# Kernel optimization log

Measured on AMD Instinct MI355X. Metric: run time of the kernel, lower is better.

## Reference

```python
import jax, jax.numpy as jnp
import numpy as np

D = 128
NHEAD = 4
HD = D // NHEAD
DFF = 2 * D
K = 3
NL = 2


def _ln(x, g, b, eps=1e-5):
    m = jnp.mean(x, axis=-1, keepdims=True)
    v = jnp.var(x, axis=-1, keepdims=True)
    return (x - m) / jnp.sqrt(v + eps) * g + b


def setup_inputs() -> dict:
    key = jax.random.key(0)
    ks = jax.random.split(key, 20)
    B, C, H, W = 2, 16, 128, 128
    inp = {
        "x": jax.random.normal(ks[0], (B, C, H, W), jnp.float32),
        "emb_w": jax.random.normal(ks[1], (D, C), jnp.float32) * (1.0 / np.sqrt(C)),
        "emb_b": jnp.zeros((D,), jnp.float32),
        "pos": jax.random.normal(ks[2], (1, K * K, D), jnp.float32) * 0.02,
        "wqkv": jax.random.normal(ks[3], (NL, 3 * D, D), jnp.float32) * (1.0 / np.sqrt(D)),
        "bqkv": jnp.zeros((NL, 3 * D), jnp.float32),
        "wo": jax.random.normal(ks[4], (NL, D, D), jnp.float32) * (1.0 / np.sqrt(D)),
        "bo": jnp.zeros((NL, D), jnp.float32),
        "ln1_g": jnp.ones((NL, D), jnp.float32),
        "ln1_b": jnp.zeros((NL, D), jnp.float32),
        "ln2_g": jnp.ones((NL, D), jnp.float32),
        "ln2_b": jnp.zeros((NL, D), jnp.float32),
        "w1": jax.random.normal(ks[5], (NL, DFF, D), jnp.float32) * (1.0 / np.sqrt(D)),
        "b1": jnp.zeros((NL, DFF), jnp.float32),
        "w2": jax.random.normal(ks[6], (NL, D, DFF), jnp.float32) * (1.0 / np.sqrt(DFF)),
        "b2": jnp.zeros((NL, D), jnp.float32),
        "lnf_g": jnp.ones((D,), jnp.float32),
        "lnf_b": jnp.zeros((D,), jnp.float32),
        "head_w": jax.random.normal(ks[7], (1, D), jnp.float32) * (1.0 / np.sqrt(D)),
        "head_b": jnp.zeros((1,), jnp.float32),
    }
    return inp


def reference(x, emb_w, emb_b, pos, wqkv, bqkv, wo, bo, ln1_g, ln1_b,
              ln2_g, ln2_b, w1, b1, w2, b2, lnf_g, lnf_b, head_w, head_b):
    B, C, H, W = x.shape
    # 1x1 conv embedding -> (B,H,W,D)
    e = jnp.einsum('bchw,dc->bhwd', x, emb_w) + emb_b
    # unfold: 3x3 windows with padding 1, kernel positions in row-major order
    ep = jnp.pad(e, ((0, 0), (1, 1), (1, 1), (0, 0)))
    wins = jnp.stack([ep[:, i:i + H, j:j + W, :]
                      for i in range(K) for j in range(K)], axis=3)  # (B,H,W,9,D)
    t = wins.reshape(B * H * W, K * K, D) + pos[0]  # (N,9,D)
    scale = 1.0 / np.sqrt(HD)

    def split_heads(a):
        return a.reshape(-1, K * K, NHEAD, HD).transpose(0, 2, 1, 3)

    for l in range(NL):
        # pre-LN self-attention
        h = _ln(t, ln1_g[l], ln1_b[l])
        qkv = h @ wqkv[l].T + bqkv[l]            # (N,9,3D)
        q, k, v = jnp.split(qkv, 3, axis=-1)
        q, k, v = split_heads(q), split_heads(k), split_heads(v)
        att = jax.nn.softmax(jnp.einsum('nhqd,nhkd->nhqk', q, k) * scale, axis=-1)
        o = jnp.einsum('nhqk,nhkd->nhqd', att, v)
        o = o.transpose(0, 2, 1, 3).reshape(-1, K * K, D)
        t = t + o @ wo[l].T + bo[l]
        # pre-LN FFN with exact GELU
        h2 = _ln(t, ln2_g[l], ln2_b[l])
        t = t + jax.nn.gelu(h2 @ w1[l].T + b1[l], approximate=False) @ w2[l].T + b2[l]

    center = t[:, (K * K) // 2, :]               # (N,D)
    center = _ln(center, lnf_g, lnf_b)
    logits = center @ head_w.T + head_b          # (N,1)
    return logits.reshape(B, H, W, 1).transpose(0, 3, 1, 2)
```

## Files before the change

kernel.cpp:

```cpp
#include <hip/hip_runtime.h>
#include <hip/hip_bf16.h>

typedef unsigned short u16;
typedef unsigned int   u32;
typedef __attribute__((ext_vector_type(8))) short bf16x8;
typedef __attribute__((ext_vector_type(4))) float f32x4;
typedef __attribute__((ext_vector_type(2))) unsigned int u32x2;

#define NTOK 32768
#define TPB  4
#define MR   36
#define MPAD 48
#define NBLK (NTOK/TPB)

#define QK_OFF 0
#define VT_OFF 24576
#define HB_OFF 40960
#define SM_ATTN 53248

__device__ __forceinline__ u16 f2bf(float f) {
    u32 u; __builtin_memcpy(&u, &f, 4);
    u32 r = (u + 0x7fffu + ((u >> 16) & 1u)) >> 16;
    return (u16)r;
}
__device__ __forceinline__ u32 packbf2(float a, float b) {
    __hip_bfloat162 h = __float22bfloat162_rn(make_float2(a, b));
    u32 r; __builtin_memcpy(&r, &h, 4); return r;
}
__device__ __forceinline__ float wredsum(float v) {
#pragma unroll
    for (int m = 32; m >= 1; m >>= 1) v += __shfl_xor(v, m, 64);
    return v;
}
__device__ __forceinline__ float gelu_f(float x) {
    float ax = fabsf(x) * 0.70710678118654752f;
    float tt = __builtin_amdgcn_rcpf(1.0f + 0.3275911f * ax);
    float poly = tt * (0.254829592f + tt * (-0.284496736f + tt * (1.421413741f +
                 tt * (-1.453152027f + tt * 1.061405429f))));
    float er = 1.0f - poly * __expf(-ax * ax);
    er = copysignf(er, x);
    return 0.5f * x * (1.0f + er);
}

__global__ __launch_bounds__(256) void k_wconv(const float* __restrict__ wqkv, const float* __restrict__ wo,
                                               const float* __restrict__ w1, const float* __restrict__ w2,
                                               u16* __restrict__ wbf) {
    int i = blockIdx.x * 256 + threadIdx.x;
    float v;
    if (i < 98304)       v = wqkv[i];
    else if (i < 131072) v = wo[i - 98304];
    else if (i < 196608) v = w1[i - 131072];
    else                 v = w2[i - 196608];
    wbf[i] = f2bf(v);
}

__global__ __launch_bounds__(256) void k_embed(const float* __restrict__ x, const float* __restrict__ ew,
                                               const float* __restrict__ eb, float* __restrict__ e) {
    int idx = blockIdx.x * 256 + threadIdx.x;
    int d = idx & 127, pix = idx >> 7;
    int b = pix >> 14, hw = pix & 16383;
    const float* xp = x + b * 262144 + hw;
    const float* wr = ew + d * 16;
    float acc = eb[d];
#pragma unroll
    for (int c = 0; c < 16; ++c) acc += xp[c * 16384] * wr[c];
    e[idx] = acc;
}

__global__ __launch_bounds__(256) void k_build(const float* __restrict__ e, const float* __restrict__ pos,
                                               float* __restrict__ t) {
    int id = blockIdx.x * 256 + threadIdx.x;
    int c4 = (id & 31) << 2;
    int np = id >> 5;
    int p = np % 9;
    int n = np / 9;
    int b = n >> 14, h = (n >> 7) & 127, w = n & 127;
    int sh = h + p / 3 - 1, sw = w + p % 3 - 1;
    float4 v = {0.f, 0.f, 0.f, 0.f};
    if (sh >= 0 && sh < 128 && sw >= 0 && sw < 128)
        v = *(const float4*)(e + (size_t)((b << 14) + (sh << 7) + sw) * 128 + c4);
    float4 pv = *(const float4*)(pos + p * 128 + c4);
    v.x += pv.x; v.y += pv.y; v.z += pv.z; v.w += pv.w;
    *(float4*)(t + (size_t)np * 128 + c4) = v;
}

__global__ __launch_bounds__(512, 6) void k_attn(
    float* __restrict__ t,
    const u16* __restrict__ wq, const float* __restrict__ bq,
    const u16* __restrict__ wov, const float* __restrict__ bov,
    const float* __restrict__ lg, const float* __restrict__ lb) {
    __shared__ char smem[SM_ATTN];
    char* qk = smem + QK_OFF;
    char* vt = smem + VT_OFF;
    char* hb = smem + HB_OFF;
    const int tid = threadIdx.x, lane = tid & 63, wid = tid >> 6;
    const int blk = blockIdx.x;
    const int col = lane & 15, grp = lane >> 4;
    const f32x4 zero4 = {0.f, 0.f, 0.f, 0.f};

    *(f32x4*)(vt + tid * 32) = zero4;
    *(f32x4*)(vt + tid * 32 + 16) = zero4;
    if (tid < 192) {
        int pr = MR + (tid >> 4), pc = (tid & 15) * 16;
        *(f32x4*)(hb + pr * 256 + (pc ^ ((pr & 7) << 4))) = zero4;
    }
    {
        float2 gv = ((const float2*)lg)[lane];
        float2 bv = ((const float2*)lb)[lane];
        for (int r = wid; r < MR; r += 8) {
            const float2* tr = (const float2*)(t + ((size_t)blk * MR + r) * 128);
            float2 xv = tr[lane];
            float mean = wredsum(xv.x + xv.y) * (1.f / 128.f);
            float var  = wredsum(xv.x * xv.x + xv.y * xv.y) * (1.f / 128.f) - mean * mean;
            float rstd = rsqrtf(var + 1e-5f);
            float h0 = (xv.x - mean) * rstd * gv.x + bv.x;
            float h1 = (xv.y - mean) * rstd * gv.y + bv.y;
            *(u32*)(hb + r * 256 + ((lane * 4) ^ ((r & 7) << 4))) = packbf2(h0, h1);
        }
    }
    __syncthreads();
    for (int nt = 0; nt < 3; ++nt) {
        int n0 = (wid * 3 + nt) * 16;
        int nr = n0 + col;
        bf16x8 bfr[4];
        const u16* wr = wq + nr * 128 + grp * 8;
#pragma unroll
        for (int ks = 0; ks < 4; ++ks) bfr[ks] = *(const bf16x8*)(wr + ks * 32);
        if (n0 < 256) {
            float scl = (n0 < 128) ? 0.17677669529663687f : 1.0f;
            float4 b4 = *(const float4*)(bq + n0 + grp * 4);
            for (int mt = 0; mt < 3; ++mt) {
                f32x4 acc = zero4;
#pragma unroll
                for (int ks = 0; ks < 4; ++ks) {
                    int row = mt * 16 + col;
                    bf16x8 a = *(const bf16x8*)(hb + row * 256 + ((ks * 64 + grp * 16) ^ ((row & 7) << 4)));
                    acc = __builtin_amdgcn_mfma_f32_16x16x32_bf16(bfr[ks], a, acc, 0, 0, 0);
                }
                int R = mt * 16 + col;
                u32x2 pk;
                pk.x = packbf2((acc[0] + b4.x) * scl, (acc[1] + b4.y) * scl);
                pk.y = packbf2((acc[2] + b4.z) * scl, (acc[3] + b4.w) * scl);
                *(u32x2*)(qk + R * 512 + (((n0 + grp * 4) * 2) ^ ((R & 7) << 4))) = pk;
            }
        } else {
            float bias = bq[nr];
            for (int mt = 0; mt < 3; ++mt) {
                f32x4 acc = zero4;
#pragma unroll
                for (int ks = 0; ks < 4; ++ks) {
                    int row = mt * 16 + col;
                    bf16x8 a = *(const bf16x8*)(hb + row * 256 + ((ks * 64 + grp * 16) ^ ((row & 7) << 4)));
                    acc = __builtin_amdgcn_mfma_f32_16x16x32_bf16(a, bfr[ks], acc, 0, 0, 0);
                }
#pragma unroll
                for (int j = 0; j < 4; ++j) {
                    int R = mt * 16 + grp * 4 + j;
                    if (R < MR) {
                        int tok = R / 9, jp = R % 9;
                        int d = nr - 256;
                        *(u16*)(vt + tok * 4096 + (jp >> 3) * 2048 + d * 16 + (jp & 7) * 2) = f2bf(acc[j] + bias);
                    }
                }
            }
        }
    }
    __syncthreads();
    for (int i = 0; i < 2; ++i) {
        int pair = wid * 2 + i;
        int tok = pair >> 2, head = pair & 3;
        int rb = tok * 9;
        int rm = rb + (col < 9 ? col : 8);
        bf16x8 kf = *(const bf16x8*)(qk + rm * 512 + ((256 + head * 64 + grp * 16) ^ ((rm & 7) << 4)));
        bf16x8 qf = *(const bf16x8*)(qk + rm * 512 + ((head * 64 + grp * 16) ^ ((rm & 7) << 4)));
        f32x4 s = __builtin_amdgcn_mfma_f32_16x16x32_bf16(kf, qf, zero4, 0, 0, 0);
        int jb = grp * 4;
        float mx = -1e30f;
#pragma unroll
        for (int r = 0; r < 4; ++r) if (jb + r < 9) mx = fmaxf(mx, s[r]);
        mx = fmaxf(mx, __shfl_xor(mx, 16, 64));
        mx = fmaxf(mx, __shfl_xor(mx, 32, 64));
        float e0[4], ss = 0.f;
#pragma unroll
        for (int r = 0; r < 4; ++r) { e0[r] = (jb + r < 9) ? __expf(s[r] - mx) : 0.f; ss += e0[r]; }
        ss += __shfl_xor(ss, 16, 64);
        ss += __shfl_xor(ss, 32, 64);
        float rinv = __builtin_amdgcn_rcpf(ss);
        u32 p0 = packbf2(e0[0] * rinv, e0[1] * rinv);
        u32 p1 = packbf2(e0[2] * rinv, e0[3] * rinv);
        int idx0 = (col + 32 * grp) * 4;
        u32 w0 = (u32)__builtin_amdgcn_ds_bpermute(idx0, (int)p0);
        u32 w1 = (u32)__builtin_amdgcn_ds_bpermute(idx0, (int)p1);
        u32 w2 = (u32)__builtin_amdgcn_ds_bpermute(idx0 + 64, (int)p0);
        u32 w3 = (u32)__builtin_amdgcn_ds_bpermute(idx0 + 64, (int)p1);
        if (grp >= 2) { w0 = 0; w1 = 0; w2 = 0; w3 = 0; }
        union { u32 w[4]; bf16x8 v; } bu;
        bu.w[0] = w0; bu.w[1] = w1; bu.w[2] = w2; bu.w[3] = w3;
#pragma unroll
        for (int dh = 0; dh < 2; ++dh) {
            bf16x8 af = *(const bf16x8*)(vt + tok * 4096 + (grp & 1) * 2048 + (head * 32 + dh * 16 + col) * 16);
            f32x4 o = __builtin_amdgcn_mfma_f32_16x16x32_bf16(af, bu.v, zero4, 0, 0, 0);
            if (col < 9) {
                int row = rb + col;
                u32x2 pk; pk.x = packbf2(o[0], o[1]); pk.y = packbf2(o[2], o[3]);
                *(u32x2*)(hb + row * 256 + ((head * 64 + dh * 32 + grp * 8) ^ ((row & 7) << 4))) = pk;
            }
        }
    }
    __syncthreads();
    {
        int n0w = wid * 16;
        int nr = n0w + col;
        bf16x8 bw[4];
        const u16* wr = wov + nr * 128 + grp * 8;
#pragma unroll
        for (int ks = 0; ks < 4; ++ks) bw[ks] = *(const bf16x8*)(wr + ks * 32);
        float4 b4 = *(const float4*)(bov + n0w + grp * 4);
        for (int mt = 0; mt < 3; ++mt) {
            f32x4 acc = zero4;
#pragma unroll
            for (int ks = 0; ks < 4; ++ks) {
                int row = mt * 16 + col;
                bf16x8 a = *(const bf16x8*)(hb + row * 256 + ((ks * 64 + grp * 16) ^ ((row & 7) << 4)));
                acc = __builtin_amdgcn_mfma_f32_16x16x32_bf16(bw[ks], a, acc, 0, 0, 0);
            }
            int R = mt * 16 + col;
            if (R < MR) {
                float* p = t + ((size_t)blk * MR + R) * 128 + n0w + grp * 4;
                float4 old = *(float4*)p;
                old.x += acc[0] + b4.x; old.y += acc[1] + b4.y;
                old.z += acc[2] + b4.z; old.w += acc[3] + b4.w;
                *(float4*)p = old;
            }
        }
    }
}

__global__ __launch_bounds__(512, 6) void k_ffn(
    float* __restrict__ t,
    const u16* __restrict__ w1w, const float* __restrict__ b1v,
    const u16* __restrict__ w2w, const float* __restrict__ b2v,
    const float* __restrict__ lg, const float* __restrict__ lb) {
    __shared__ char smem[36864];
    char* hb  = smem;
    char* mid = smem + 12288;
    const int tid = threadIdx.x, lane = tid & 63, wid = tid >> 6;
    const int blk = blockIdx.x;
    const int col = lane & 15, grp = lane >> 4;
    const f32x4 zero4 = {0.f, 0.f, 0.f, 0.f};

    if (tid < 192) {
        int pr = MR + (tid >> 4), pc = (tid & 15) * 16;
        *(f32x4*)(hb + pr * 256 + (pc ^ ((pr & 7) << 4))) = zero4;
    }
    {
        float2 gv = ((const float2*)lg)[lane];
        float2 bv = ((const float2*)lb)[lane];
        for (int r = wid; r < MR; r += 8) {
            const float2* tr = (const float2*)(t + ((size_t)blk * MR + r) * 128);
            float2 xv = tr[lane];
            float mean = wredsum(xv.x + xv.y) * (1.f / 128.f);
            float var  = wredsum(xv.x * xv.x + xv.y * xv.y) * (1.f / 128.f) - mean * mean;
            float rstd = rsqrtf(var + 1e-5f);
            float h0 = (xv.x - mean) * rstd * gv.x + bv.x;
            float h1 = (xv.y - mean) * rstd * gv.y + bv.y;
            *(u32*)(hb + r * 256 + ((lane * 4) ^ ((r & 7) << 4))) = packbf2(h0, h1);
        }
    }
    __syncthreads();
    for (int nt = 0; nt < 2; ++nt) {
        int n0 = (wid * 2 + nt) * 16;
        int nr = n0 + col;
        bf16x8 bfr[4];
        const u16* wr = w1w + nr * 128 + grp * 8;
#pragma unroll
        for (int ks = 0; ks < 4; ++ks) bfr[ks] = *(const bf16x8*)(wr + ks * 32);
        float4 b4 = *(const float4*)(b1v + n0 + grp * 4);
        for (int mt = 0; mt < 3; ++mt) {
            f32x4 acc = zero4;
#pragma unroll
            for (int ks = 0; ks < 4; ++ks) {
                int row = mt * 16 + col;
                bf16x8 a = *(const bf16x8*)(hb + row * 256 + ((ks * 64 + grp * 16) ^ ((row & 7) << 4)));
                acc = __builtin_amdgcn_mfma_f32_16x16x32_bf16(bfr[ks], a, acc, 0, 0, 0);
            }
            int R = mt * 16 + col;
            float g0 = gelu_f(acc[0] + b4.x), g1 = gelu_f(acc[1] + b4.y);
            float g2 = gelu_f(acc[2] + b4.z), g3 = gelu_f(acc[3] + b4.w);
            u32x2 pk; pk.x = packbf2(g0, g1); pk.y = packbf2(g2, g3);
            *(u32x2*)(mid + R * 512 + (((n0 + grp * 4) * 2) ^ ((R & 7) << 4))) = pk;
        }
    }
    __syncthreads();
    {
        int n0w = wid * 16;
        int nr = n0w + col;
        bf16x8 bfr[8];
        const u16* wr = w2w + nr * 256 + grp * 8;
#pragma unroll
        for (int ks = 0; ks < 8; ++ks) bfr[ks] = *(const bf16x8*)(wr + ks * 32);
        float4 b4 = *(const float4*)(b2v + n0w + grp * 4);
        for (int mt = 0; mt < 3; ++mt) {
            f32x4 acc = zero4;
#pragma unroll
            for (int ks = 0; ks < 8; ++ks) {
                int row = mt * 16 + col;
                bf16x8 a = *(const bf16x8*)(mid + row * 512 + ((ks * 64 + grp * 16) ^ ((row & 7) << 4)));
                acc = __builtin_amdgcn_mfma_f32_16x16x32_bf16(bfr[ks], a, acc, 0, 0, 0);
            }
            int R = mt * 16 + col;
            if (R < MR) {
                float* p = t + ((size_t)blk * MR + R) * 128 + n0w + grp * 4;
                float4 old = *(float4*)p;
                old.x += acc[0] + b4.x; old.y += acc[1] + b4.y;
                old.z += acc[2] + b4.z; old.w += acc[3] + b4.w;
                *(float4*)p = old;
            }
        }
    }
}

__global__ __launch_bounds__(256) void k_head(const float* __restrict__ t, const float* __restrict__ g,
                                              const float* __restrict__ b, const float* __restrict__ hw,
                                              const float* __restrict__ hbias, float* __restrict__ out) {
    int lane = threadIdx.x & 63, wid = threadIdx.x >> 6;
    int base = blockIdx.x * 16 + wid * 4;
    float2 gv = ((const float2*)g)[lane];
    float2 bv = ((const float2*)b)[lane];
    float2 wv = ((const float2*)hw)[lane];
    float hb0 = hbias[0];
    for (int it = 0; it < 4; ++it) {
        int n = base + it;
        const float2* row = (const float2*)(t + ((size_t)n * 9 + 4) * 128);
        float2 xv = row[lane];
        float mean = wredsum(xv.x + xv.y) * (1.f / 128.f);
        float var  = wredsum(xv.x * xv.x + xv.y * xv.y) * (1.f / 128.f) - mean * mean;
        float rstd = rsqrtf(var + 1e-5f);
        float v = ((xv.x - mean) * rstd * gv.x + bv.x) * wv.x +
                  ((xv.y - mean) * rstd * gv.y + bv.y) * wv.y;
        v = wredsum(v);
        if (lane == 0) out[n] = v + hb0;
    }
}

extern "C" void kernel_launch(void* const* d_in, const int* in_sizes, int n_in,
                              void* d_out, int out_size, void* d_ws, size_t ws_size,
                              hipStream_t stream) {
    (void)in_sizes; (void)n_in; (void)out_size; (void)ws_size;
    const float* x     = (const float*)d_in[0];
    const float* emb_w = (const float*)d_in[1];
    const float* emb_b = (const float*)d_in[2];
    const float* pos   = (const float*)d_in[3];
    const float* wqkv  = (const float*)d_in[4];
    const float* bqkv  = (const float*)d_in[5];
    const float* wo    = (const float*)d_in[6];
    const float* bo    = (const float*)d_in[7];
    const float* ln1g  = (const float*)d_in[8];
    const float* ln1b  = (const float*)d_in[9];
    const float* ln2g  = (const float*)d_in[10];
    const float* ln2b  = (const float*)d_in[11];
    const float* w1    = (const float*)d_in[12];
    const float* b1    = (const float*)d_in[13];
    const float* w2    = (const float*)d_in[14];
    const float* b2    = (const float*)d_in[15];
    const float* lnfg  = (const float*)d_in[16];
    const float* lnfb  = (const float*)d_in[17];
    const float* headw = (const float*)d_in[18];
    const float* headb = (const float*)d_in[19];
    float* out = (float*)d_out;

    char* ws = (char*)d_ws;
    float* e = (float*)ws;
    float* t = (float*)(ws + 16777216);
    u16* wbf = (u16*)(ws + 167772160);

    k_wconv<<<1024, 256, 0, stream>>>(wqkv, wo, w1, w2, wbf);
    k_embed<<<16384, 256, 0, stream>>>(x, emb_w, emb_b, e);
    k_build<<<36864, 256, 0, stream>>>(e, pos, t);
    for (int l = 0; l < 2; ++l) {
        k_attn<<<NBLK, 512, 0, stream>>>(t, wbf + l * 49152, bqkv + l * 384,
                                         wbf + 98304 + l * 16384, bo + l * 128,
                                         ln1g + l * 128, ln1b + l * 128);
        k_ffn<<<NBLK, 512, 0, stream>>>(t, wbf + 131072 + l * 32768, b1 + l * 256,
                                        wbf + 196608 + l * 32768, b2 + l * 128,
                                        ln2g + l * 128, ln2b + l * 128);
    }
    k_head<<<2048, 256, 0, stream>>>(t, lnfg, lnfb, headw, headb, out);
}
```

Baseline: 895.5 us.

## Fuse window build into first attention and head into last FFN

Drops the separate unfold/build kernel: the first attention layer gathers 3x3 window tokens from the embedding directly and adds positional encodings while computing LN1. It also writes the token tensor for later use. The head (final LN plus projection) is folded into the last FFN, which skips writing the full token tensor and keeps only centre tokens in LDS. Residual values are prefetched into registers at kernel start, which adds register pressure.

```diff
diff --git a/kernel.cpp b/kernel.cpp
--- a/kernel.cpp
+++ b/kernel.cpp
@@ -58,8 +58,8 @@
                                                const float* __restrict__ eb, float* __restrict__ e) {
     int idx = blockIdx.x * 256 + threadIdx.x;
     int d = idx & 127, pix = idx >> 7;
-    int b = pix >> 14, hw = pix & 16383;
-    const float* xp = x + b * 262144 + hw;
+    int b = pix >> 14, hw2 = pix & 16383;
+    const float* xp = x + b * 262144 + hw2;
     const float* wr = ew + d * 16;
     float acc = eb[d];
 #pragma unroll
@@ -67,25 +67,9 @@
     e[idx] = acc;
 }
 
-__global__ __launch_bounds__(256) void k_build(const float* __restrict__ e, const float* __restrict__ pos,
-                                               float* __restrict__ t) {
-    int id = blockIdx.x * 256 + threadIdx.x;
-    int c4 = (id & 31) << 2;
-    int np = id >> 5;
-    int p = np % 9;
-    int n = np / 9;
-    int b = n >> 14, h = (n >> 7) & 127, w = n & 127;
-    int sh = h + p / 3 - 1, sw = w + p % 3 - 1;
-    float4 v = {0.f, 0.f, 0.f, 0.f};
-    if (sh >= 0 && sh < 128 && sw >= 0 && sw < 128)
-        v = *(const float4*)(e + (size_t)((b << 14) + (sh << 7) + sw) * 128 + c4);
-    float4 pv = *(const float4*)(pos + p * 128 + c4);
-    v.x += pv.x; v.y += pv.y; v.z += pv.z; v.w += pv.w;
-    *(float4*)(t + (size_t)np * 128 + c4) = v;
-}
-
+template<int FIRST>
 __global__ __launch_bounds__(512, 6) void k_attn(
-    float* __restrict__ t,
+    float* __restrict__ t, const float* __restrict__ e, const float* __restrict__ pos,
     const u16* __restrict__ wq, const float* __restrict__ bq,
     const u16* __restrict__ wov, const float* __restrict__ bov,
     const float* __restrict__ lg, const float* __restrict__ lb) {
@@ -98,6 +82,14 @@
     const int col = lane & 15, grp = lane >> 4;
     const f32x4 zero4 = {0.f, 0.f, 0.f, 0.f};
 
+    float4 tpre[3];
+    if (!FIRST) {
+#pragma unroll
+        for (int mt = 0; mt < 3; ++mt) {
+            int R = mt * 16 + col;
+            if (R < MR) tpre[mt] = *(const float4*)(t + ((size_t)blk * MR + R) * 128 + wid * 16 + grp * 4);
+        }
+    }
     *(f32x4*)(vt + tid * 32) = zero4;
     *(f32x4*)(vt + tid * 32 + 16) = zero4;
     if (tid < 192) {
@@ -108,8 +100,21 @@
         float2 gv = ((const float2*)lg)[lane];
         float2 bv = ((const float2*)lb)[lane];
         for (int r = wid; r < MR; r += 8) {
-            const float2* tr = (const float2*)(t + ((size_t)blk * MR + r) * 128);
-            float2 xv = tr[lane];
+            float2 xv;
+            if (FIRST) {
+                int tl = r / 9, p = r % 9;
+                int n = blk * TPB + tl;
+                int b = n >> 14, hh = (n >> 7) & 127, ww = n & 127;
+                int sh = hh + p / 3 - 1, sw = ww + p % 3 - 1;
+                if (sh >= 0 && sh < 128 && sw >= 0 && sw < 128)
+                    xv = ((const float2*)(e + (size_t)((b << 14) + (sh << 7) + sw) * 128))[lane];
+                else { xv.x = 0.f; xv.y = 0.f; }
+                float2 pv = ((const float2*)(pos + p * 128))[lane];
+                xv.x += pv.x; xv.y += pv.y;
+                ((float2*)(t + ((size_t)blk * MR + r) * 128))[lane] = xv;
+            } else {
+                xv = ((const float2*)(t + ((size_t)blk * MR + r) * 128))[lane];
+            }
             float mean = wredsum(xv.x + xv.y) * (1.f / 128.f);
             float var  = wredsum(xv.x * xv.x + xv.y * xv.y) * (1.f / 128.f) - mean * mean;
             float rstd = rsqrtf(var + 1e-5f);
@@ -119,6 +124,13 @@
         }
     }
     __syncthreads();
+    if (FIRST) {
+#pragma unroll
+        for (int mt = 0; mt < 3; ++mt) {
+            int R = mt * 16 + col;
+            if (R < MR) tpre[mt] = *(const float4*)(t + ((size_t)blk * MR + R) * 128 + wid * 16 + grp * 4);
+        }
+    }
     for (int nt = 0; nt < 3; ++nt) {
         int n0 = (wid * 3 + nt) * 16;
         int nr = n0 + col;
@@ -227,7 +239,7 @@
             int R = mt * 16 + col;
             if (R < MR) {
                 float* p = t + ((size_t)blk * MR + R) * 128 + n0w + grp * 4;
-                float4 old = *(float4*)p;
+                float4 old = tpre[mt];
                 old.x += acc[0] + b4.x; old.y += acc[1] + b4.y;
                 old.z += acc[2] + b4.z; old.w += acc[3] + b4.w;
                 *(float4*)p = old;
@@ -236,19 +248,30 @@
     }
 }
 
+template<int LAST>
 __global__ __launch_bounds__(512, 6) void k_ffn(
     float* __restrict__ t,
     const u16* __restrict__ w1w, const float* __restrict__ b1v,
     const u16* __restrict__ w2w, const float* __restrict__ b2v,
-    const float* __restrict__ lg, const float* __restrict__ lb) {
+    const float* __restrict__ lg, const float* __restrict__ lb,
+    const float* __restrict__ lnfg, const float* __restrict__ lnfb,
+    const float* __restrict__ hwv, const float* __restrict__ hbias,
+    float* __restrict__ outp) {
     __shared__ char smem[36864];
     char* hb  = smem;
     char* mid = smem + 12288;
+    char* hlds = smem;
     const int tid = threadIdx.x, lane = tid & 63, wid = tid >> 6;
     const int blk = blockIdx.x;
     const int col = lane & 15, grp = lane >> 4;
     const f32x4 zero4 = {0.f, 0.f, 0.f, 0.f};
 
+    float4 tpre[3];
+#pragma unroll
+    for (int mt = 0; mt < 3; ++mt) {
+        int R = mt * 16 + col;
+        if (R < MR) tpre[mt] = *(const float4*)(t + ((size_t)blk * MR + R) * 128 + wid * 16 + grp * 4);
+    }
     if (tid < 192) {
         int pr = MR + (tid >> 4), pc = (tid & 15) * 16;
         *(f32x4*)(hb + pr * 256 + (pc ^ ((pr & 7) << 4))) = zero4;
@@ -310,36 +333,32 @@
             }
             int R = mt * 16 + col;
             if (R < MR) {
-                float* p = t + ((size_t)blk * MR + R) * 128 + n0w + grp * 4;
-                float4 old = *(float4*)p;
+                float4 old = tpre[mt];
                 old.x += acc[0] + b4.x; old.y += acc[1] + b4.y;
                 old.z += acc[2] + b4.z; old.w += acc[3] + b4.w;
-                *(float4*)p = old;
-            }
-        }
-    }
-}
-
-__global__ __launch_bounds__(256) void k_head(const float* __restrict__ t, const float* __restrict__ g,
-                                              const float* __restrict__ b, const float* __restrict__ hw,
-                                              const float* __restrict__ hbias, float* __restrict__ out) {
-    int lane = threadIdx.x & 63, wid = threadIdx.x >> 6;
-    int base = blockIdx.x * 16 + wid * 4;
-    float2 gv = ((const float2*)g)[lane];
-    float2 bv = ((const float2*)b)[lane];
-    float2 wv = ((const float2*)hw)[lane];
-    float hb0 = hbias[0];
-    for (int it = 0; it < 4; ++it) {
-        int n = base + it;
-        const float2* row = (const float2*)(t + ((size_t)n * 9 + 4) * 128);
-        float2 xv = row[lane];
-        float mean = wredsum(xv.x + xv.y) * (1.f / 128.f);
-        float var  = wredsum(xv.x * xv.x + xv.y * xv.y) * (1.f / 128.f) - mean * mean;
-        float rstd = rsqrtf(var + 1e-5f);
-        float v = ((xv.x - mean) * rstd * gv.x + bv.x) * wv.x +
-                  ((xv.y - mean) * rstd * gv.y + bv.y) * wv.y;
-        v = wredsum(v);
-        if (lane == 0) out[n] = v + hb0;
+                if (!LAST) {
+                    *(float4*)(t + ((size_t)blk * MR + R) * 128 + n0w + grp * 4) = old;
+                } else if (R % 9 == 4) {
+                    *(float4*)(hlds + (R / 9) * 512 + (n0w + grp * 4) * 4) = old;
+                }
+            }
+        }
+    }
+    if (LAST) {
+        __syncthreads();
+        if (wid < 4) {
+            float2 xv = ((const float2*)(hlds + wid * 512))[lane];
+            float mean = wredsum(xv.x + xv.y) * (1.f / 128.f);
+            float var  = wredsum(xv.x * xv.x + xv.y * xv.y) * (1.f / 128.f) - mean * mean;
+            float rstd = rsqrtf(var + 1e-5f);
+            float2 gv = ((const float2*)lnfg)[lane];
+            float2 bv = ((const float2*)lnfb)[lane];
+            float2 wv = ((const float2*)hwv)[lane];
+            float v = ((xv.x - mean) * rstd * gv.x + bv.x) * wv.x +
+                      ((xv.y - mean) * rstd * gv.y + bv.y) * wv.y;
+            v = wredsum(v);
+            if (lane == 0) outp[blk * TPB + wid] = v + hbias[0];
+        }
     }
 }
 
@@ -376,14 +395,12 @@
 
     k_wconv<<<1024, 256, 0, stream>>>(wqkv, wo, w1, w2, wbf);
     k_embed<<<16384, 256, 0, stream>>>(x, emb_w, emb_b, e);
-    k_build<<<36864, 256, 0, stream>>>(e, pos, t);
-    for (int l = 0; l < 2; ++l) {
-        k_attn<<<NBLK, 512, 0, stream>>>(t, wbf + l * 49152, bqkv + l * 384,
-                                         wbf + 98304 + l * 16384, bo + l * 128,
-                                         ln1g + l * 128, ln1b + l * 128);
-        k_ffn<<<NBLK, 512, 0, stream>>>(t, wbf + 131072 + l * 32768, b1 + l * 256,
-                                        wbf + 196608 + l * 32768, b2 + l * 128,
-                                        ln2g + l * 128, ln2b + l * 128);
-    }
-    k_head<<<2048, 256, 0, stream>>>(t, lnfg, lnfb, headw, headb, out);
-}
+    k_attn<1><<<NBLK, 512, 0, stream>>>(t, e, pos, wbf, bqkv,
+                                        wbf + 98304, bo, ln1g, ln1b);
+    k_ffn<0><<<NBLK, 512, 0, stream>>>(t, wbf + 131072, b1, wbf + 196608, b2,
+                                       ln2g, ln2b, nullptr, nullptr, nullptr, nullptr, nullptr);
+    k_attn<0><<<NBLK, 512, 0, stream>>>(t, nullptr, nullptr, wbf + 49152, bqkv + 384,
+                                        wbf + 98304 + 16384, bo + 128, ln1g + 128, ln1b + 128);
+    k_ffn<1><<<NBLK, 512, 0, stream>>>(t, wbf + 131072 + 32768, b1 + 256, wbf + 196608 + 32768, b2 + 128,
+                                       ln2g + 128, ln2b + 128, lnfg, lnfb, headw, headb, out);
+}
```

Result: slower. 1.008 ms (+12.6%).
